# Optimization experiments

Measured on AMD Instinct MI355X. Metric: run time of the kernel, lower is better.

The kernel has to match this reference:

```python
import jax, jax.numpy as jnp
import numpy as np

EPS = 1e-5  # torch LayerNorm default


def setup_inputs() -> dict:
    key = jax.random.key(0)
    ks = jax.random.split(key, 16)
    B, S, E = 2, 2048, 1024
    H, DK, DV = 16, 64, 64
    s_in = 1.0 / np.sqrt(E)
    s_ctx = 1.0 / np.sqrt(H * DV)
    return {
        "Q": jax.random.normal(ks[0], (B, S, E), jnp.float32),
        "K": jax.random.normal(ks[1], (B, S, E), jnp.float32),
        "V": jax.random.normal(ks[2], (B, S, E), jnp.float32),
        "attn_mask": jax.random.randint(ks[3], (B, S, S), 0, 2).astype(bool),
        "Wq": jax.random.normal(ks[4], (E, H * DK), jnp.float32) * s_in,
        "bq": jnp.zeros((H * DK,), jnp.float32),
        "Wk": jax.random.normal(ks[5], (E, H * DK), jnp.float32) * s_in,
        "bk": jnp.zeros((H * DK,), jnp.float32),
        "Wv": jax.random.normal(ks[6], (E, H * DV), jnp.float32) * s_in,
        "bv": jnp.zeros((H * DV,), jnp.float32),
        "Wo": jax.random.normal(ks[7], (H * DV, E), jnp.float32) * s_ctx,
        "bo": jnp.zeros((E,), jnp.float32),
        "gamma": jnp.ones((E,), jnp.float32),
        "beta": jnp.zeros((E,), jnp.float32),
        "n_heads": 16,
        "d_k": 64,
        "d_v": 64,
    }


def reference(Q, K, V, attn_mask, Wq, bq, Wk, bk, Wv, bv, Wo, bo, gamma, beta,
              n_heads, d_k, d_v):
    B, S, E = Q.shape
    # QKV projections -> [B, H, S, d]
    q = (Q @ Wq + bq).reshape(B, S, n_heads, d_k).transpose(0, 2, 1, 3)
    k = (K @ Wk + bk).reshape(B, S, n_heads, d_k).transpose(0, 2, 1, 3)
    v = (V @ Wv + bv).reshape(B, S, n_heads, d_v).transpose(0, 2, 1, 3)
    # scaled dot-product attention with explicit [B,H,S,S] scores
    scores = jnp.einsum('bhqd,bhkd->bhqk', q, k) / np.sqrt(d_k).astype(jnp.float32)
    scores = jnp.where(attn_mask[:, None, :, :], jnp.float32(-1e9), scores)
    attn = jax.nn.softmax(scores, axis=-1)
    context = jnp.einsum('bhqk,bhkd->bhqd', attn, v)
    context = context.transpose(0, 2, 1, 3).reshape(B, S, n_heads * d_v)
    output = context @ Wo + bo
    # residual + LayerNorm over last dim
    x = output + Q
    mu = jnp.mean(x, axis=-1, keepdims=True)
    var = jnp.mean(jnp.square(x - mu), axis=-1, keepdims=True)
    y = (x - mu) * jax.lax.rsqrt(var + EPS) * gamma + beta
    return (y, attn)
```

## Files before the change

kernel.cpp:

```cpp
#include <hip/hip_runtime.h>
#include <cstdint>
#include <cstddef>

#define Bc 2
#define Sc 2048
#define Ec 1024
#define Hc 16
#define Dc 64
#define BSc 4096
#define BHc 32

typedef __attribute__((ext_vector_type(8))) short bf16x8;
typedef __attribute__((ext_vector_type(4))) float f32x4;

__device__ __forceinline__ uint16_t f2b(float x) {
  union { float f; uint32_t u; } v; v.f = x;
  return (uint16_t)((v.u + 0x7FFFu + ((v.u >> 16) & 1u)) >> 16);
}

__device__ __forceinline__ uint4 pack8(const float* f) {
  union { uint16_t u[8]; uint4 v; } pk;
#pragma unroll
  for (int i = 0; i < 8; i++) pk.u[i] = f2b(f[i]);
  return pk.v;
}

__global__ void conv_bf16(const float* __restrict__ src, uint16_t* __restrict__ dst, int n) {
  int i = (blockIdx.x * blockDim.x + threadIdx.x) * 4;
  if (i < n) {
    float4 v = *(const float4*)(src + i);
    ushort4 o;
    o.x = f2b(v.x); o.y = f2b(v.y); o.z = f2b(v.z); o.w = f2b(v.w);
    *(ushort4*)(dst + i) = o;
  }
}

__global__ void transpose_bf16(const float* __restrict__ src, uint16_t* __restrict__ dst) {
  __shared__ uint16_t tile[32][33];
  int x0 = blockIdx.x * 32, y0 = blockIdx.y * 32;
  int tx = threadIdx.x & 31, ty = threadIdx.x >> 5;
#pragma unroll
  for (int i = 0; i < 32; i += 8)
    tile[ty + i][tx] = f2b(src[(size_t)(y0 + ty + i) * 1024 + x0 + tx]);
  __syncthreads();
#pragma unroll
  for (int i = 0; i < 32; i += 8)
    dst[(size_t)(x0 + ty + i) * 1024 + y0 + tx] = tile[tx][ty + i];
}

__global__ __launch_bounds__(256) void gemm_proj(
    const uint16_t* __restrict__ A, const uint16_t* __restrict__ BT,
    const float* __restrict__ bias, uint16_t* __restrict__ out, int mode) {
  const int K = 1024;
  __shared__ uint16_t As[128 * 40];
  __shared__ uint16_t Bs[128 * 40];
  int n0 = blockIdx.x * 128, m0 = blockIdx.y * 128;
  int t = threadIdx.x;
  int wave = t >> 6, lane = t & 63;
  int wm = (wave >> 1) * 64, wn = (wave & 1) * 64;
  int quad = lane >> 4, l16 = lane & 15;

  f32x4 acc[4][4];
#pragma unroll
  for (int i = 0; i < 4; i++)
#pragma unroll
    for (int j = 0; j < 4; j++) acc[i][j] = (f32x4)(0.0f);

  int srow = t >> 1, scol = (t & 1) * 16;

  for (int k0 = 0; k0 < K; k0 += 32) {
    const uint16_t* ag = A + (size_t)(m0 + srow) * K + k0 + scol;
    const uint16_t* bg = BT + (size_t)(n0 + srow) * K + k0 + scol;
    uint4 av0 = *(const uint4*)ag;
    uint4 av1 = *(const uint4*)(ag + 8);
    uint4 bv0 = *(const uint4*)bg;
    uint4 bv1 = *(const uint4*)(bg + 8);
    __syncthreads();
    *(uint4*)(As + srow * 40 + scol) = av0;
    *(uint4*)(As + srow * 40 + scol + 8) = av1;
    *(uint4*)(Bs + srow * 40 + scol) = bv0;
    *(uint4*)(Bs + srow * 40 + scol + 8) = bv1;
    __syncthreads();
    bf16x8 af[4], bfr[4];
#pragma unroll
    for (int i = 0; i < 4; i++)
      af[i] = *(const bf16x8*)(As + (wm + i * 16 + l16) * 40 + quad * 8);
#pragma unroll
    for (int j = 0; j < 4; j++)
      bfr[j] = *(const bf16x8*)(Bs + (wn + j * 16 + l16) * 40 + quad * 8);
#pragma unroll
    for (int i = 0; i < 4; i++)
#pragma unroll
      for (int j = 0; j < 4; j++)
        acc[i][j] = __builtin_amdgcn_mfma_f32_16x16x32_bf16(af[i], bfr[j], acc[i][j], 0, 0, 0);
  }
#pragma unroll
  for (int i = 0; i < 4; i++)
#pragma unroll
    for (int j = 0; j < 4; j++) {
      int col = n0 + wn + j * 16 + l16;
      float bval = bias[col];
      int h = col >> 6, d = col & 63;
#pragma unroll
      for (int r = 0; r < 4; r++) {
        int row = m0 + wm + i * 16 + quad * 4 + r;
        int b = row >> 11, s = row & 2047;
        uint16_t hv = f2b(acc[i][j][r] + bval);
        if (mode == 0)
          out[(size_t)((b * Hc + h) * Sc + s) * Dc + d] = hv;
        else
          out[(size_t)((b * Hc + h) * Dc + d) * Sc + s] = hv;
      }
    }
}

__global__ __launch_bounds__(256) void gemm_out(
    const uint16_t* __restrict__ A, const uint16_t* __restrict__ BT,
    const float* __restrict__ bias, const float* __restrict__ resid,
    float* __restrict__ x) {
  const int K = 1024;
  __shared__ uint16_t As[128 * 40];
  __shared__ uint16_t Bs[128 * 40];
  int n0 = blockIdx.x * 128, m0 = blockIdx.y * 128;
  int t = threadIdx.x;
  int wave = t >> 6, lane = t & 63;
  int wm = (wave >> 1) * 64, wn = (wave & 1) * 64;
  int quad = lane >> 4, l16 = lane & 15;

  f32x4 acc[4][4];
#pragma unroll
  for (int i = 0; i < 4; i++)
#pragma unroll
    for (int j = 0; j < 4; j++) acc[i][j] = (f32x4)(0.0f);

  int srow = t >> 1, scol = (t & 1) * 16;
  for (int k0 = 0; k0 < K; k0 += 32) {
    const uint16_t* ag = A + (size_t)(m0 + srow) * K + k0 + scol;
    const uint16_t* bg = BT + (size_t)(n0 + srow) * K + k0 + scol;
    uint4 av0 = *(const uint4*)ag;
    uint4 av1 = *(const uint4*)(ag + 8);
    uint4 bv0 = *(const uint4*)bg;
    uint4 bv1 = *(const uint4*)(bg + 8);
    __syncthreads();
    *(uint4*)(As + srow * 40 + scol) = av0;
    *(uint4*)(As + srow * 40 + scol + 8) = av1;
    *(uint4*)(Bs + srow * 40 + scol) = bv0;
    *(uint4*)(Bs + srow * 40 + scol + 8) = bv1;
    __syncthreads();
    bf16x8 af[4], bfr[4];
#pragma unroll
    for (int i = 0; i < 4; i++)
      af[i] = *(const bf16x8*)(As + (wm + i * 16 + l16) * 40 + quad * 8);
#pragma unroll
    for (int j = 0; j < 4; j++)
      bfr[j] = *(const bf16x8*)(Bs + (wn + j * 16 + l16) * 40 + quad * 8);
#pragma unroll
    for (int i = 0; i < 4; i++)
#pragma unroll
      for (int j = 0; j < 4; j++)
        acc[i][j] = __builtin_amdgcn_mfma_f32_16x16x32_bf16(af[i], bfr[j], acc[i][j], 0, 0, 0);
  }
#pragma unroll
  for (int i = 0; i < 4; i++)
#pragma unroll
    for (int j = 0; j < 4; j++) {
      int col = n0 + wn + j * 16 + l16;
      float bval = bias[col];
#pragma unroll
      for (int r = 0; r < 4; r++) {
        int row = m0 + wm + i * 16 + quad * 4 + r;
        x[(size_t)row * 1024 + col] = acc[i][j][r] + bval + resid[(size_t)row * 1024 + col];
      }
    }
}

__global__ __launch_bounds__(256) void scores_kernel(
    const uint16_t* __restrict__ q,
    const uint16_t* __restrict__ k,
    const int* __restrict__ mask,
    float* __restrict__ attn,
    float* __restrict__ rowsum) {
  __shared__ uint16_t Qs[128 * 72];
  __shared__ uint16_t Ks[128 * 72];
  int n0 = blockIdx.x * 128, m0 = blockIdx.y * 128;
  int bh = blockIdx.z;
  int b = bh >> 4;
  int t = threadIdx.x;
  int wave = t >> 6, lane = t & 63;
  int wm = (wave >> 1) * 64, wn = (wave & 1) * 64;
  int quad = lane >> 4, l16 = lane & 15;

  int srow = t >> 1, scol = (t & 1) * 32;
  {
    const uint16_t* qg = q + (size_t)(bh * Sc + m0 + srow) * Dc + scol;
    const uint16_t* kg = k + (size_t)(bh * Sc + n0 + srow) * Dc + scol;
#pragma unroll
    for (int c = 0; c < 4; c++)
      *(uint4*)(Qs + srow * 72 + scol + c * 8) = *(const uint4*)(qg + c * 8);
#pragma unroll
    for (int c = 0; c < 4; c++)
      *(uint4*)(Ks + srow * 72 + scol + c * 8) = *(const uint4*)(kg + c * 8);
  }
  __syncthreads();

  f32x4 acc[4][4];
#pragma unroll
  for (int i = 0; i < 4; i++)
#pragma unroll
    for (int j = 0; j < 4; j++) acc[i][j] = (f32x4)(0.0f);

#pragma unroll
  for (int kk = 0; kk < 2; kk++) {
    bf16x8 af[4], bfr[4];
#pragma unroll
    for (int i = 0; i < 4; i++)
      af[i] = *(const bf16x8*)(Qs + (wm + i * 16 + l16) * 72 + kk * 32 + quad * 8);
#pragma unroll
    for (int j = 0; j < 4; j++)
      bfr[j] = *(const bf16x8*)(Ks + (wn + j * 16 + l16) * 72 + kk * 32 + quad * 8);
#pragma unroll
    for (int i = 0; i < 4; i++)
#pragma unroll
      for (int j = 0; j < 4; j++)
        acc[i][j] = __builtin_amdgcn_mfma_f32_16x16x32_bf16(af[i], bfr[j], acc[i][j], 0, 0, 0);
  }

#pragma unroll
  for (int i = 0; i < 4; i++) {
#pragma unroll
    for (int r = 0; r < 4; r++) {
      int m = m0 + wm + i * 16 + quad * 4 + r;
      const int* mrow = mask + (size_t)(b * Sc + m) * Sc;
      float* arow = attn + ((size_t)(bh * Sc + m)) * Sc;
      float rs = 0.0f;
#pragma unroll
      for (int j = 0; j < 4; j++) {
        int n = n0 + wn + j * 16 + l16;
        float sc = acc[i][j][r] * 0.125f;
        float p = mrow[n] ? 0.0f : __expf(sc);
        arow[n] = p;
        rs += p;
      }
      rs += __shfl_xor(rs, 1);
      rs += __shfl_xor(rs, 2);
      rs += __shfl_xor(rs, 4);
      rs += __shfl_xor(rs, 8);
      if (l16 == 0) atomicAdd(&rowsum[bh * Sc + m], rs);
    }
  }
}

__global__ void inv_kernel(const float* __restrict__ rowsum, float* __restrict__ rowinv, int n) {
  int i = blockIdx.x * blockDim.x + threadIdx.x;
  if (i < n) rowinv[i] = 1.0f / rowsum[i];
}

__global__ __launch_bounds__(256) void context_kernel(
    float* __restrict__ attn,
    const float* __restrict__ rowinv,
    const uint16_t* __restrict__ vT,
    uint16_t* __restrict__ ctx) {
  __shared__ uint16_t As[64 * 72];
  __shared__ uint16_t Vs[64 * 72];
  int m0 = blockIdx.x * 64;
  int bh = blockIdx.y;
  int t = threadIdx.x;
  int wave = t >> 6, lane = t & 63;
  int quad = lane >> 4, l16 = lane & 15;

  f32x4 acc[4];
#pragma unroll
  for (int j = 0; j < 4; j++) acc[j] = (f32x4)(0.0f);

  int arow = t >> 2, acol = (t & 3) * 16;
  float inv_r = rowinv[bh * Sc + m0 + arow];
  int vrow = t >> 2, vcol = (t & 3) * 16;

  for (int k0 = 0; k0 < Sc; k0 += 64) {
    float* ag = attn + ((size_t)(bh * Sc + m0 + arow)) * Sc + k0 + acol;
    float va[16];
    float4 a0 = *(const float4*)ag;
    float4 a1 = *(const float4*)(ag + 4);
    float4 a2 = *(const float4*)(ag + 8);
    float4 a3 = *(const float4*)(ag + 12);
    va[0] = a0.x * inv_r;  va[1] = a0.y * inv_r;  va[2] = a0.z * inv_r;  va[3] = a0.w * inv_r;
    va[4] = a1.x * inv_r;  va[5] = a1.y * inv_r;  va[6] = a1.z * inv_r;  va[7] = a1.w * inv_r;
    va[8] = a2.x * inv_r;  va[9] = a2.y * inv_r;  va[10] = a2.z * inv_r; va[11] = a2.w * inv_r;
    va[12] = a3.x * inv_r; va[13] = a3.y * inv_r; va[14] = a3.z * inv_r; va[15] = a3.w * inv_r;
    float4 w0 = make_float4(va[0], va[1], va[2], va[3]);
    float4 w1 = make_float4(va[4], va[5], va[6], va[7]);
    float4 w2 = make_float4(va[8], va[9], va[10], va[11]);
    float4 w3 = make_float4(va[12], va[13], va[14], va[15]);
    *(float4*)ag = w0;
    *(float4*)(ag + 4) = w1;
    *(float4*)(ag + 8) = w2;
    *(float4*)(ag + 12) = w3;
    const uint16_t* vg = vT + ((size_t)(bh * Dc + vrow)) * Sc + k0 + vcol;
    uint4 vv0 = *(const uint4*)vg;
    uint4 vv1 = *(const uint4*)(vg + 8);
    __syncthreads();
    *(uint4*)(As + arow * 72 + acol) = pack8(va);
    *(uint4*)(As + arow * 72 + acol + 8) = pack8(va + 8);
    *(uint4*)(Vs + vrow * 72 + vcol) = vv0;
    *(uint4*)(Vs + vrow * 72 + vcol + 8) = vv1;
    __syncthreads();
#pragma unroll
    for (int kk = 0; kk < 2; kk++) {
      bf16x8 af = *(const bf16x8*)(As + (wave * 16 + l16) * 72 + kk * 32 + quad * 8);
#pragma unroll
      for (int j = 0; j < 4; j++) {
        bf16x8 bfr = *(const bf16x8*)(Vs + (j * 16 + l16) * 72 + kk * 32 + quad * 8);
        acc[j] = __builtin_amdgcn_mfma_f32_16x16x32_bf16(af, bfr, acc[j], 0, 0, 0);
      }
    }
    __syncthreads();
  }
  int b = bh >> 4, h = bh & 15;
#pragma unroll
  for (int j = 0; j < 4; j++) {
    int d = j * 16 + l16;
#pragma unroll
    for (int r = 0; r < 4; r++) {
      int s = m0 + wave * 16 + quad * 4 + r;
      ctx[(size_t)(b * Sc + s) * (Hc * Dc) + h * Dc + d] = f2b(acc[j][r]);
    }
  }
}

__global__ __launch_bounds__(256) void ln_kernel(
    const float* __restrict__ x, const float* __restrict__ gamma,
    const float* __restrict__ beta, float* __restrict__ y) {
  int row = blockIdx.x;
  int t = threadIdx.x;
  const float* xr = x + (size_t)row * 1024;
  float4 v = *(const float4*)(xr + t * 4);
  float s = v.x + v.y + v.z + v.w;
  float s2 = v.x * v.x + v.y * v.y + v.z * v.z + v.w * v.w;
#pragma unroll
  for (int o = 1; o < 64; o <<= 1) {
    s += __shfl_xor(s, o);
    s2 += __shfl_xor(s2, o);
  }
  __shared__ float ss[4], ss2[4];
  int wave = t >> 6, lane = t & 63;
  if (lane == 0) { ss[wave] = s; ss2[wave] = s2; }
  __syncthreads();
  s = ss[0] + ss[1] + ss[2] + ss[3];
  s2 = ss2[0] + ss2[1] + ss2[2] + ss2[3];
  float mu = s * (1.0f / 1024.0f);
  float var = s2 * (1.0f / 1024.0f) - mu * mu;
  float rstd = rsqrtf(var + 1e-5f);
  float4 g = *(const float4*)(gamma + t * 4);
  float4 be = *(const float4*)(beta + t * 4);
  float4 o;
  o.x = (v.x - mu) * rstd * g.x + be.x;
  o.y = (v.y - mu) * rstd * g.y + be.y;
  o.z = (v.z - mu) * rstd * g.z + be.z;
  o.w = (v.w - mu) * rstd * g.w + be.w;
  *(float4*)(y + (size_t)row * 1024 + t * 4) = o;
}

extern "C" void kernel_launch(void* const* d_in, const int* in_sizes, int n_in,
                              void* d_out, int out_size, void* d_ws, size_t ws_size,
                              hipStream_t stream) {
  const float* Q = (const float*)d_in[0];
  const float* K = (const float*)d_in[1];
  const float* V = (const float*)d_in[2];
  const int* mask = (const int*)d_in[3];
  const float* Wq = (const float*)d_in[4];
  const float* bq = (const float*)d_in[5];
  const float* Wk = (const float*)d_in[6];
  const float* bk = (const float*)d_in[7];
  const float* Wv = (const float*)d_in[8];
  const float* bv = (const float*)d_in[9];
  const float* Wo = (const float*)d_in[10];
  const float* bo = (const float*)d_in[11];
  const float* gamma = (const float*)d_in[12];
  const float* beta = (const float*)d_in[13];

  float* y = (float*)d_out;
  float* attn = (float*)d_out + (size_t)BSc * Ec;

  char* ws = (char*)d_ws;
  size_t off = 0;
  auto alloc = [&](size_t bytes) -> void* {
    void* p = ws + off;
    off = (off + bytes + 255) & ~(size_t)255;
    return p;
  };
  uint16_t* Qb  = (uint16_t*)alloc((size_t)BSc * Ec * 2);
  uint16_t* Kb  = (uint16_t*)alloc((size_t)BSc * Ec * 2);
  uint16_t* Vb  = (uint16_t*)alloc((size_t)BSc * Ec * 2);
  uint16_t* WqT = (uint16_t*)alloc((size_t)Ec * Ec * 2);
  uint16_t* WkT = (uint16_t*)alloc((size_t)Ec * Ec * 2);
  uint16_t* WvT = (uint16_t*)alloc((size_t)Ec * Ec * 2);
  uint16_t* WoT = (uint16_t*)alloc((size_t)Ec * Ec * 2);
  uint16_t* qh  = (uint16_t*)alloc((size_t)BHc * Sc * Dc * 2);
  uint16_t* kh  = (uint16_t*)alloc((size_t)BHc * Sc * Dc * 2);
  uint16_t* vT  = (uint16_t*)alloc((size_t)BHc * Dc * Sc * 2);
  uint16_t* ctx = (uint16_t*)alloc((size_t)BSc * Ec * 2);
  float* xres   = (float*)alloc((size_t)BSc * Ec * 4);
  float* rowsum = (float*)alloc((size_t)BHc * Sc * 4);
  float* rowinv = (float*)alloc((size_t)BHc * Sc * 4);

  const int n_qkv = BSc * Ec;

  conv_bf16<<<n_qkv / 1024, 256, 0, stream>>>(Q, Qb, n_qkv);
  conv_bf16<<<n_qkv / 1024, 256, 0, stream>>>(K, Kb, n_qkv);
  conv_bf16<<<n_qkv / 1024, 256, 0, stream>>>(V, Vb, n_qkv);
  dim3 tg(32, 32);
  transpose_bf16<<<tg, 256, 0, stream>>>(Wq, WqT);
  transpose_bf16<<<tg, 256, 0, stream>>>(Wk, WkT);
  transpose_bf16<<<tg, 256, 0, stream>>>(Wv, WvT);
  transpose_bf16<<<tg, 256, 0, stream>>>(Wo, WoT);
  dim3 pg(Ec / 128, BSc / 128);
  gemm_proj<<<pg, 256, 0, stream>>>(Qb, WqT, bq, qh, 0);
  gemm_proj<<<pg, 256, 0, stream>>>(Kb, WkT, bk, kh, 0);
  gemm_proj<<<pg, 256, 0, stream>>>(Vb, WvT, bv, vT, 1);
  hipMemsetAsync(rowsum, 0, (size_t)BHc * Sc * 4, stream);
  dim3 sg(Sc / 128, Sc / 128, BHc);
  scores_kernel<<<sg, 256, 0, stream>>>(qh, kh, mask, attn, rowsum);
  inv_kernel<<<(BHc * Sc) / 256, 256, 0, stream>>>(rowsum, rowinv, BHc * Sc);
  dim3 cg(Sc / 64, BHc);
  context_kernel<<<cg, 256, 0, stream>>>(attn, rowinv, vT, ctx);
  gemm_out<<<pg, 256, 0, stream>>>(ctx, WoT, bo, Q, xres);
  ln_kernel<<<BSc, 256, 0, stream>>>(xres, gamma, beta, y);
}
```

Measured before the change: 1.115 ms.

## Store unnormalized scores as bf16 and write final fp32 attn once in context kernel

The scores kernel now loops over all key tiles per query block, writes unnormalized exp values as bf16 to a scratch buffer, and computes row sums in shared memory. This removes the global atomics, the memset and the separate inverse kernel. The context kernel reads the bf16 P, writes the normalized fp32 attention once, and applies 1/rowsum to the context accumulator instead of the inputs. The goal is to avoid the fp32 attn read-modify-write round trip, at the cost of a large bf16 scratch buffer and much less grid parallelism in the scores kernel (512 blocks instead of 8192). The returned attn values now carry bf16 rounding.

```diff
diff --git a/kernel.cpp b/kernel.cpp
--- a/kernel.cpp
+++ b/kernel.cpp
@@ -18,11 +18,10 @@
   return (uint16_t)((v.u + 0x7FFFu + ((v.u >> 16) & 1u)) >> 16);
 }
 
-__device__ __forceinline__ uint4 pack8(const float* f) {
-  union { uint16_t u[8]; uint4 v; } pk;
-#pragma unroll
-  for (int i = 0; i < 8; i++) pk.u[i] = f2b(f[i]);
-  return pk.v;
+__device__ __forceinline__ void unpack2(uint32_t u, float& lo, float& hi) {
+  union { uint32_t u; float f; } a, b;
+  a.u = u << 16; b.u = u & 0xFFFF0000u;
+  lo = a.f; hi = b.f;
 }
 
 __global__ void conv_bf16(const float* __restrict__ src, uint16_t* __restrict__ dst, int n) {
@@ -178,12 +177,14 @@
     const uint16_t* __restrict__ q,
     const uint16_t* __restrict__ k,
     const int* __restrict__ mask,
-    float* __restrict__ attn,
-    float* __restrict__ rowsum) {
+    uint16_t* __restrict__ P,
+    float* __restrict__ rowinv) {
   __shared__ uint16_t Qs[128 * 72];
   __shared__ uint16_t Ks[128 * 72];
-  int n0 = blockIdx.x * 128, m0 = blockIdx.y * 128;
-  int bh = blockIdx.z;
+  __shared__ uint16_t Ps[128 * 136];
+  __shared__ float rowsum_s[128];
+  int m0 = blockIdx.x * 128;
+  int bh = blockIdx.y;
   int b = bh >> 4;
   int t = threadIdx.x;
   int wave = t >> 6, lane = t & 63;
@@ -193,136 +194,176 @@
   int srow = t >> 1, scol = (t & 1) * 32;
   {
     const uint16_t* qg = q + (size_t)(bh * Sc + m0 + srow) * Dc + scol;
-    const uint16_t* kg = k + (size_t)(bh * Sc + n0 + srow) * Dc + scol;
 #pragma unroll
     for (int c = 0; c < 4; c++)
       *(uint4*)(Qs + srow * 72 + scol + c * 8) = *(const uint4*)(qg + c * 8);
-#pragma unroll
-    for (int c = 0; c < 4; c++)
-      *(uint4*)(Ks + srow * 72 + scol + c * 8) = *(const uint4*)(kg + c * 8);
+  }
+  if (t < 128) rowsum_s[t] = 0.0f;
+
+  float rs[4][4];
+#pragma unroll
+  for (int i = 0; i < 4; i++)
+#pragma unroll
+    for (int r = 0; r < 4; r++) rs[i][r] = 0.0f;
+
+  for (int n0 = 0; n0 < Sc; n0 += 128) {
+    __syncthreads();
+    {
+      const uint16_t* kg = k + (size_t)(bh * Sc + n0 + srow) * Dc + scol;
+#pragma unroll
+      for (int c = 0; c < 4; c++)
+        *(uint4*)(Ks + srow * 72 + scol + c * 8) = *(const uint4*)(kg + c * 8);
+    }
+    __syncthreads();
+
+    f32x4 acc[4][4];
+#pragma unroll
+    for (int i = 0; i < 4; i++)
+#pragma unroll
+      for (int j = 0; j < 4; j++) acc[i][j] = (f32x4)(0.0f);
+#pragma unroll
+    for (int kk = 0; kk < 2; kk++) {
+      bf16x8 af[4], bfr[4];
+#pragma unroll
+      for (int i = 0; i < 4; i++)
+        af[i] = *(const bf16x8*)(Qs + (wm + i * 16 + l16) * 72 + kk * 32 + quad * 8);
+#pragma unroll
+      for (int j = 0; j < 4; j++)
+        bfr[j] = *(const bf16x8*)(Ks + (wn + j * 16 + l16) * 72 + kk * 32 + quad * 8);
+#pragma unroll
+      for (int i = 0; i < 4; i++)
+#pragma unroll
+        for (int j = 0; j < 4; j++)
+          acc[i][j] = __builtin_amdgcn_mfma_f32_16x16x32_bf16(af[i], bfr[j], acc[i][j], 0, 0, 0);
+    }
+
+#pragma unroll
+    for (int i = 0; i < 4; i++) {
+#pragma unroll
+      for (int r = 0; r < 4; r++) {
+        int mloc = wm + i * 16 + quad * 4 + r;
+        const int* mrow = mask + (size_t)(b * Sc + m0 + mloc) * Sc + n0;
+#pragma unroll
+        for (int j = 0; j < 4; j++) {
+          int cloc = wn + j * 16 + l16;
+          float sc = acc[i][j][r] * 0.125f;
+          float p = mrow[cloc] ? 0.0f : __expf(sc);
+          rs[i][r] += p;
+          Ps[mloc * 136 + cloc] = f2b(p);
+        }
+      }
+    }
+    __syncthreads();
+    {
+      int row = t >> 1, half = (t & 1) * 64;
+      uint16_t* pg = P + (size_t)(bh * Sc + m0 + row) * Sc + n0 + half;
+#pragma unroll
+      for (int c = 0; c < 8; c++)
+        *(uint4*)(pg + c * 8) = *(const uint4*)(Ps + row * 136 + half + c * 8);
+    }
+  }
+
+#pragma unroll
+  for (int i = 0; i < 4; i++) {
+#pragma unroll
+    for (int r = 0; r < 4; r++) {
+      float v = rs[i][r];
+      v += __shfl_xor(v, 1);
+      v += __shfl_xor(v, 2);
+      v += __shfl_xor(v, 4);
+      v += __shfl_xor(v, 8);
+      if (l16 == 0) atomicAdd(&rowsum_s[wm + i * 16 + quad * 4 + r], v);
+    }
   }
   __syncthreads();
-
-  f32x4 acc[4][4];
-#pragma unroll
-  for (int i = 0; i < 4; i++)
-#pragma unroll
-    for (int j = 0; j < 4; j++) acc[i][j] = (f32x4)(0.0f);
-
-#pragma unroll
-  for (int kk = 0; kk < 2; kk++) {
-    bf16x8 af[4], bfr[4];
-#pragma unroll
-    for (int i = 0; i < 4; i++)
-      af[i] = *(const bf16x8*)(Qs + (wm + i * 16 + l16) * 72 + kk * 32 + quad * 8);
-#pragma unroll
-    for (int j = 0; j < 4; j++)
-      bfr[j] = *(const bf16x8*)(Ks + (wn + j * 16 + l16) * 72 + kk * 32 + quad * 8);
-#pragma unroll
-    for (int i = 0; i < 4; i++)
-#pragma unroll
-      for (int j = 0; j < 4; j++)
-        acc[i][j] = __builtin_amdgcn_mfma_f32_16x16x32_bf16(af[i], bfr[j], acc[i][j], 0, 0, 0);
-  }
-
-#pragma unroll
-  for (int i = 0; i < 4; i++) {
-#pragma unroll
-    for (int r = 0; r < 4; r++) {
-      int m = m0 + wm + i * 16 + quad * 4 + r;
-      const int* mrow = mask + (size_t)(b * Sc + m) * Sc;
-      float* arow = attn + ((size_t)(bh * Sc + m)) * Sc;
-      float rs = 0.0f;
-#pragma unroll
-      for (int j = 0; j < 4; j++) {
-        int n = n0 + wn + j * 16 + l16;
-        float sc = acc[i][j][r] * 0.125f;
-        float p = mrow[n] ? 0.0f : __expf(sc);
-        arow[n] = p;
-        rs += p;
-      }
-      rs += __shfl_xor(rs, 1);
-      rs += __shfl_xor(rs, 2);
-      rs += __shfl_xor(rs, 4);
-      rs += __shfl_xor(rs, 8);
-      if (l16 == 0) atomicAdd(&rowsum[bh * Sc + m], rs);
-    }
-  }
-}
-
-__global__ void inv_kernel(const float* __restrict__ rowsum, float* __restrict__ rowinv, int n) {
-  int i = blockIdx.x * blockDim.x + threadIdx.x;
-  if (i < n) rowinv[i] = 1.0f / rowsum[i];
+  if (t < 128) rowinv[bh * Sc + m0 + t] = 1.0f / rowsum_s[t];
 }
 
 __global__ __launch_bounds__(256) void context_kernel(
-    float* __restrict__ attn,
+    const uint16_t* __restrict__ P,
     const float* __restrict__ rowinv,
     const uint16_t* __restrict__ vT,
+    float* __restrict__ attn,
     uint16_t* __restrict__ ctx) {
-  __shared__ uint16_t As[64 * 72];
-  __shared__ uint16_t Vs[64 * 72];
-  int m0 = blockIdx.x * 64;
+  __shared__ uint16_t Ps[128 * 136];
+  __shared__ uint16_t Vs[64 * 136];
+  int m0 = blockIdx.x * 128;
   int bh = blockIdx.y;
   int t = threadIdx.x;
   int wave = t >> 6, lane = t & 63;
   int quad = lane >> 4, l16 = lane & 15;
 
-  f32x4 acc[4];
-#pragma unroll
-  for (int j = 0; j < 4; j++) acc[j] = (f32x4)(0.0f);
-
-  int arow = t >> 2, acol = (t & 3) * 16;
-  float inv_r = rowinv[bh * Sc + m0 + arow];
-  int vrow = t >> 2, vcol = (t & 3) * 16;
-
-  for (int k0 = 0; k0 < Sc; k0 += 64) {
-    float* ag = attn + ((size_t)(bh * Sc + m0 + arow)) * Sc + k0 + acol;
-    float va[16];
-    float4 a0 = *(const float4*)ag;
-    float4 a1 = *(const float4*)(ag + 4);
-    float4 a2 = *(const float4*)(ag + 8);
-    float4 a3 = *(const float4*)(ag + 12);
-    va[0] = a0.x * inv_r;  va[1] = a0.y * inv_r;  va[2] = a0.z * inv_r;  va[3] = a0.w * inv_r;
-    va[4] = a1.x * inv_r;  va[5] = a1.y * inv_r;  va[6] = a1.z * inv_r;  va[7] = a1.w * inv_r;
-    va[8] = a2.x * inv_r;  va[9] = a2.y * inv_r;  va[10] = a2.z * inv_r; va[11] = a2.w * inv_r;
-    va[12] = a3.x * inv_r; va[13] = a3.y * inv_r; va[14] = a3.z * inv_r; va[15] = a3.w * inv_r;
-    float4 w0 = make_float4(va[0], va[1], va[2], va[3]);
-    float4 w1 = make_float4(va[4], va[5], va[6], va[7]);
-    float4 w2 = make_float4(va[8], va[9], va[10], va[11]);
-    float4 w3 = make_float4(va[12], va[13], va[14], va[15]);
-    *(float4*)ag = w0;
-    *(float4*)(ag + 4) = w1;
-    *(float4*)(ag + 8) = w2;
-    *(float4*)(ag + 12) = w3;
-    const uint16_t* vg = vT + ((size_t)(bh * Dc + vrow)) * Sc + k0 + vcol;
-    uint4 vv0 = *(const uint4*)vg;
-    uint4 vv1 = *(const uint4*)(vg + 8);
-    __syncthreads();
-    *(uint4*)(As + arow * 72 + acol) = pack8(va);
-    *(uint4*)(As + arow * 72 + acol + 8) = pack8(va + 8);
-    *(uint4*)(Vs + vrow * 72 + vcol) = vv0;
-    *(uint4*)(Vs + vrow * 72 + vcol + 8) = vv1;
-    __syncthreads();
-#pragma unroll
-    for (int kk = 0; kk < 2; kk++) {
-      bf16x8 af = *(const bf16x8*)(As + (wave * 16 + l16) * 72 + kk * 32 + quad * 8);
+  int prow = t >> 1, phalf = (t & 1) * 64;
+  float inv_r = rowinv[bh * Sc + m0 + prow];
+  int vrow = t >> 2, vcol = (t & 3) * 32;
+
+  f32x4 acc[2][4];
+#pragma unroll
+  for (int i = 0; i < 2; i++)
+#pragma unroll
+    for (int j = 0; j < 4; j++) acc[i][j] = (f32x4)(0.0f);
+
+  for (int k0 = 0; k0 < Sc; k0 += 128) {
+    const uint16_t* pg = P + (size_t)(bh * Sc + m0 + prow) * Sc + k0 + phalf;
+    uint4 pv[8];
+#pragma unroll
+    for (int c = 0; c < 8; c++) pv[c] = *(const uint4*)(pg + c * 8);
+    const uint16_t* vg = vT + (size_t)(bh * Dc + vrow) * Sc + k0 + vcol;
+    uint4 vv[4];
+#pragma unroll
+    for (int c = 0; c < 4; c++) vv[c] = *(const uint4*)(vg + c * 8);
+
+    __syncthreads();
+#pragma unroll
+    for (int c = 0; c < 8; c++) *(uint4*)(Ps + prow * 136 + phalf + c * 8) = pv[c];
+#pragma unroll
+    for (int c = 0; c < 4; c++) *(uint4*)(Vs + vrow * 136 + vcol + c * 8) = vv[c];
+    __syncthreads();
+
+    {
+      float* arow = attn + (size_t)(bh * Sc + m0 + prow) * Sc + k0 + phalf;
+#pragma unroll
+      for (int c = 0; c < 8; c++) {
+        float f[8];
+        unpack2(pv[c].x, f[0], f[1]);
+        unpack2(pv[c].y, f[2], f[3]);
+        unpack2(pv[c].z, f[4], f[5]);
+        unpack2(pv[c].w, f[6], f[7]);
+        float4 w0 = make_float4(f[0] * inv_r, f[1] * inv_r, f[2] * inv_r, f[3] * inv_r);
+        float4 w1 = make_float4(f[4] * inv_r, f[5] * inv_r, f[6] * inv_r, f[7] * inv_r);
+        *(float4*)(arow + c * 8) = w0;
+        *(float4*)(arow + c * 8 + 4) = w1;
+      }
+    }
+
+#pragma unroll
+    for (int kk = 0; kk < 4; kk++) {
+      bf16x8 af[2];
+#pragma unroll
+      for (int i = 0; i < 2; i++)
+        af[i] = *(const bf16x8*)(Ps + (wave * 32 + i * 16 + l16) * 136 + kk * 32 + quad * 8);
 #pragma unroll
       for (int j = 0; j < 4; j++) {
-        bf16x8 bfr = *(const bf16x8*)(Vs + (j * 16 + l16) * 72 + kk * 32 + quad * 8);
-        acc[j] = __builtin_amdgcn_mfma_f32_16x16x32_bf16(af, bfr, acc[j], 0, 0, 0);
-      }
-    }
-    __syncthreads();
-  }
+        bf16x8 bfr = *(const bf16x8*)(Vs + (j * 16 + l16) * 136 + kk * 32 + quad * 8);
+#pragma unroll
+        for (int i = 0; i < 2; i++)
+          acc[i][j] = __builtin_amdgcn_mfma_f32_16x16x32_bf16(af[i], bfr, acc[i][j], 0, 0, 0);
+      }
+    }
+  }
+
   int b = bh >> 4, h = bh & 15;
 #pragma unroll
-  for (int j = 0; j < 4; j++) {
-    int d = j * 16 + l16;
+  for (int i = 0; i < 2; i++) {
 #pragma unroll
     for (int r = 0; r < 4; r++) {
-      int s = m0 + wave * 16 + quad * 4 + r;
-      ctx[(size_t)(b * Sc + s) * (Hc * Dc) + h * Dc + d] = f2b(acc[j][r]);
+      int m = m0 + wave * 32 + i * 16 + quad * 4 + r;
+      float iv = rowinv[bh * Sc + m];
+#pragma unroll
+      for (int j = 0; j < 4; j++) {
+        int d = j * 16 + l16;
+        ctx[(size_t)(b * Sc + m) * (Hc * Dc) + h * Dc + d] = f2b(acc[i][j][r] * iv);
+      }
     }
   }
 }
@@ -400,8 +441,8 @@
   uint16_t* vT  = (uint16_t*)alloc((size_t)BHc * Dc * Sc * 2);
   uint16_t* ctx = (uint16_t*)alloc((size_t)BSc * Ec * 2);
   float* xres   = (float*)alloc((size_t)BSc * Ec * 4);
-  float* rowsum = (float*)alloc((size_t)BHc * Sc * 4);
   float* rowinv = (float*)alloc((size_t)BHc * Sc * 4);
+  uint16_t* Pws = (uint16_t*)alloc((size_t)BHc * Sc * Sc * 2);
 
   const int n_qkv = BSc * Ec;
 
@@ -417,12 +458,10 @@
   gemm_proj<<<pg, 256, 0, stream>>>(Qb, WqT, bq, qh, 0);
   gemm_proj<<<pg, 256, 0, stream>>>(Kb, WkT, bk, kh, 0);
   gemm_proj<<<pg, 256, 0, stream>>>(Vb, WvT, bv, vT, 1);
-  hipMemsetAsync(rowsum, 0, (size_t)BHc * Sc * 4, stream);
-  dim3 sg(Sc / 128, Sc / 128, BHc);
-  scores_kernel<<<sg, 256, 0, stream>>>(qh, kh, mask, attn, rowsum);
-  inv_kernel<<<(BHc * Sc) / 256, 256, 0, stream>>>(rowsum, rowinv, BHc * Sc);
-  dim3 cg(Sc / 64, BHc);
-  context_kernel<<<cg, 256, 0, stream>>>(attn, rowinv, vT, ctx);
+  dim3 sg(Sc / 128, BHc);
+  scores_kernel<<<sg, 256, 0, stream>>>(qh, kh, mask, Pws, rowinv);
+  dim3 cg(Sc / 128, BHc);
+  context_kernel<<<cg, 256, 0, stream>>>(Pws, rowinv, vT, attn, ctx);
   gemm_out<<<pg, 256, 0, stream>>>(ctx, WoT, bo, Q, xres);
   ln_kernel<<<BSc, 256, 0, stream>>>(xres, gamma, beta, y);
 }
```

Result: slower. 1.249 ms (+12.0%).
